# Optimization experiments

Hardware: AMD Instinct MI355X
Metric: run time of the kernel (lower is better)

Reference implementation:

```python
import jax, jax.numpy as jnp
import numpy as np

N_NODES = 100000
N_EDGES = 1600000
D_IN = 128
D_OUT = 128
EPS = 1e-12  # F.normalize default eps


def setup_inputs() -> dict:
    key = jax.random.key(0)
    k1, k2, k3, k4 = jax.random.split(key, 4)
    h = jax.random.normal(k1, (N_NODES, D_IN), dtype=jnp.float32)
    # torch Linear(in_feats*2, out_feats): weight [out, 2*in]
    W = jax.random.normal(k2, (D_OUT, 2 * D_IN), dtype=jnp.float32) * (1.0 / np.sqrt(2 * D_IN))
    b = jnp.zeros((D_OUT,), dtype=jnp.float32)
    edge_src = jax.random.randint(k3, (N_EDGES,), 0, N_NODES, dtype=jnp.int64 if jax.config.jax_enable_x64 else jnp.int32)
    edge_dst = jax.random.randint(k4, (N_EDGES,), 0, N_NODES, dtype=jnp.int64 if jax.config.jax_enable_x64 else jnp.int32)
    return {"h": h, "W": W, "b": b, "edge_src": edge_src, "edge_dst": edge_dst}


def reference(h, W, b, edge_src, edge_dst):
    # message passing: m_e = h[src_e]; mean-reduce by dst node
    msgs = h[edge_src]                                            # [E, D]
    summed = jax.ops.segment_sum(msgs, edge_dst, num_segments=N_NODES)
    deg = jax.ops.segment_sum(jnp.ones((edge_dst.shape[0],), h.dtype),
                              edge_dst, num_segments=N_NODES)
    c = summed / jnp.maximum(deg, 1.0)[:, None]                   # mean aggregate
    # Bundler: concat -> linear -> L2 normalize -> relu
    bundle = jnp.concatenate([h, c], axis=1) @ W.T + b            # [N, D_OUT]
    norm = jnp.linalg.norm(bundle, axis=1, keepdims=True)
    bundle = bundle / jnp.maximum(norm, EPS)
    return jax.nn.relu(bundle)
```

## Files before the change

### kernel.cpp

```cpp
#include <hip/hip_runtime.h>
#include <hip/hip_bf16.h>

#define NN 100000
#define NE 1600000
#define DF 128
#define NB 1563
#define NCB 196
#define P1B 512
#define CHUNK 3125
#define CELLCAP 48
#define CAP 48
#define XP2 132

typedef unsigned char u8;
typedef unsigned short u16;
typedef unsigned int u32;
typedef __attribute__((ext_vector_type(8))) short short8;
typedef __attribute__((ext_vector_type(4))) float f32x4;

__device__ __forceinline__ u16 f2bf(float f) {
    __hip_bfloat16 x = __float2bfloat16(f);
    return *reinterpret_cast<u16*>(&x);
}


__global__ void cast_w(const float* __restrict__ W, u16* __restrict__ Wb) {
    int i = blockIdx.x * 256 + threadIdx.x;
    int o = i >> 8;
    int p = i & 255;
    int base = p & 128;
    int ph = p & 127;
    int f = (ph >> 1) + ((ph & 1) << 6);
    Wb[i] = f2bf(W[o * 256 + base + f]);
}

__global__ void cast_h(const float* __restrict__ h, u16* __restrict__ hb) {
    int i = blockIdx.x * 256 + threadIdx.x;
    int r = i >> 4;
    int pc = (i & 15) * 8;
    const float* hr = h + (size_t)r * DF;
    int fb = pc >> 1;
    float4 a = *(const float4*)(hr + fb);
    float4 b = *(const float4*)(hr + fb + 64);
    union { u16 s[8]; uint4 v; } u;
    u.s[0] = f2bf(a.x); u.s[1] = f2bf(b.x);
    u.s[2] = f2bf(a.y); u.s[3] = f2bf(b.y);
    u.s[4] = f2bf(a.z); u.s[5] = f2bf(b.z);
    u.s[6] = f2bf(a.w); u.s[7] = f2bf(b.w);
    *(uint4*)(hb + (size_t)i * 8) = u.v;
}

__global__ void __launch_bounds__(256)
bucket_fill(const int* __restrict__ esrc, const int* __restrict__ edst,
            u32* __restrict__ bkt, u8* __restrict__ gcnt2) {
    __shared__ __align__(16) u32 lbuf[NCB * 32];
    __shared__ int cnt[NCB], flushed[NCB];
    __shared__ u32 q[128];
    __shared__ int qn;

    const int t = threadIdx.x;
    const int b = blockIdx.x;
    for (int i = t; i < NCB; i += 256) { cnt[i] = 0; flushed[i] = 0; }
    if (t == 0) qn = 0;
    __syncthreads();

    const int e0 = b * CHUNK, e1 = e0 + CHUNK;
    int e = e0 + t;
    bool val = e < e1;
    int dc = 0, sc = 0;
    if (val) { dc = edst[e]; sc = esrc[e]; }

    for (int base = e0; base < e1; base += 256) {
        int en = base + 256 + t;
        bool valn = en < e1;
        int dn = 0, sn = 0;
        if (valn) { dn = edst[en]; sn = esrc[en]; }

        if (val) {
            int d = dc; d = (d < 0) ? 0 : ((d >= NN) ? NN - 1 : d);
            int s = sc; s = (s < 0) ? 0 : ((s >= NN) ? NN - 1 : s);
            int cb = d >> 9;
            u32 entry = (u32)s | ((u32)(d & 511) << 17);
            int p = atomicAdd(&cnt[cb], 1);
            lbuf[cb * 32 + (p & 31)] = entry;
        }
        __syncthreads();
        if (t < NCB) {
            int ntask = (cnt[t] - flushed[t]) >> 4;
            for (int k = 0; k < ntask; ++k) {
                int f = flushed[t];
                if (f <= CELLCAP - 16) {
                    int slot = atomicAdd(&qn, 1);
                    q[slot & 127] = ((u32)t << 3) | (u32)(f >> 4);
                }
                flushed[t] = f + 16;
            }
        }
        __syncthreads();
        int nq = qn; if (nq > 128) nq = 128;
        if (t < nq * 4) {
            u32 task = q[t >> 2];
            int bk = (int)(task >> 3);
            int f  = (int)(task & 7) << 4;
            int part = t & 3;
            uint4 v = *(const uint4*)(lbuf + bk * 32 + (f & 31) + part * 4);
            *(uint4*)(bkt + ((size_t)b * NCB + bk) * CELLCAP + f + part * 4) = v;
        }
        __syncthreads();
        if (t == 0) qn = 0;
        dc = dn; sc = sn; val = valn;
    }
    if (t < NCB) {
        int c = cnt[t], f = flushed[t];
        if (c > f && f <= CELLCAP - 16) {
            u32* dst = bkt + ((size_t)b * NCB + t) * CELLCAP + f;
            const u32* src = lbuf + t * 32 + (f & 31);
            #pragma unroll
            for (int p = 0; p < 4; ++p) *(uint4*)(dst + p * 4) = *(const uint4*)(src + p * 4);
        }
        gcnt2[t * P1B + b] = (u8)((c > CELLCAP) ? CELLCAP : c);
    }
}

__global__ void __launch_bounds__(512)
rebin(const u32* __restrict__ bkt_in, const u8* __restrict__ gcnt2,
      u32* __restrict__ bkt, u8* __restrict__ deg) {
    extern __shared__ __align__(16) u32 smem[];
    u32* csr = smem;
    int* wcur = (int*)(smem + 512 * CAP);

    const int t = threadIdx.x;
    const int cb = blockIdx.x;
    if (t < 512) wcur[t] = 0;
    __syncthreads();

    {
        int cw = (int)gcnt2[cb * P1B + t];
        const u32* cell = bkt_in + ((size_t)t * NCB + cb) * CELLCAP;
        for (int i = 0; i < cw; i += 4) {
            uint4 v = *(const uint4*)(cell + i);
            u32 ee[4] = {v.x, v.y, v.z, v.w};
            #pragma unroll
            for (int j = 0; j < 4; ++j) {
                if (i + j < cw) {
                    u32 en = ee[j];
                    int ld = (int)(en >> 17);
                    int pos = atomicAdd(&wcur[ld], 1);
                    if (pos < CAP) csr[ld * CAP + pos] = en & 0x1FFFFu;
                }
            }
        }
    }
    __syncthreads();

    {
        int n = wcur[t]; if (n > CAP) n = CAP;
        u32* c = csr + t * CAP;
        for (int i = 1; i < n; ++i) {
            u32 key = c[i];
            int j = i - 1;
            while (j >= 0 && c[j] > key) { c[j + 1] = c[j]; --j; }
            c[j + 1] = key;
        }
        int node = cb * 512 + t;
        if (node < NN) deg[node] = (u8)n;
    }
    __syncthreads();

    for (int i = t; i < 512 * CAP / 4; i += 512) {
        int cell = i / 12, off = i % 12;
        *(uint4*)(bkt + ((size_t)cell * NCB + cb) * CELLCAP + off * 4) =
            ((const uint4*)csr)[i];
    }
}

__global__ void __launch_bounds__(256)
sage_fused(const u16* __restrict__ hb, const u8* __restrict__ deg,
           const u32* __restrict__ bkt, const u16* __restrict__ Wb,
           const float* __restrict__ bias, float* __restrict__ out) {
    __shared__ __align__(16) u16 xm[64 * XP2];
    u32* nbr = (u32*)xm;
    int* dgl = (int*)(xm + 64 * 96);

    const int t = threadIdx.x;

    const int x = blockIdx.x & 7;
    const int seq = blockIdx.x >> 3;
    const int cb = x + 8 * (seq >> 3);
    if (cb >= NCB) return;
    const int sl = cb * 8 + (seq & 7);
    if (sl >= NB) return;
    const int node0 = sl * 64;
    const int j0 = (seq & 7) * 64;

    {
        const int n = t >> 2, part = t & 3;
        const u32* cell = bkt + ((size_t)(j0 + n) * NCB + cb) * CELLCAP;
        uint4* dst = (uint4*)(nbr + n * CAP);
        #pragma unroll
        for (int k = 0; k < 3; ++k)
            dst[part * 3 + k] = *(const uint4*)(cell + part * 12 + k * 4);
    }
    if (t < 64) {
        int node = node0 + t;
        dgl[t] = (node < NN) ? (int)deg[node] : 0;
    }
    __syncthreads();

    const int grp = t >> 2;
    const int sub = t & 3;
    const int dg = dgl[grp];

    float a[32];
    #pragma unroll
    for (int i = 0; i < 32; ++i) a[i] = 0.f;
    {
        const u32* nrow = nbr + grp * CAP;
        int src = (dg > 0) ? (int)nrow[0] : 0;
        for (int p = 0; p < dg; ++p) {
            int nsrc = (p + 1 < dg) ? (int)nrow[p + 1] : 0;
            const uint4* hp = (const uint4*)((const u32*)hb + (size_t)src * 64 + sub * 16);
            #pragma unroll
            for (int qq = 0; qq < 4; ++qq) {
                uint4 v = hp[qq];
                u32 wv[4] = {v.x, v.y, v.z, v.w};
                #pragma unroll
                for (int m = 0; m < 4; ++m) {
                    union { u32 i; float f; } lo, hi;
                    lo.i = wv[m] << 16;
                    hi.i = wv[m] & 0xFFFF0000u;
                    a[qq * 8 + m * 2 + 0] += lo.f;
                    a[qq * 8 + m * 2 + 1] += hi.f;
                }
            }
            src = nsrc;
        }
    }

    float rinv = 1.0f / fmaxf((float)dg, 1.0f);
    __syncthreads();
    {
        u16* dstm = xm + grp * XP2 + sub * 32;
        #pragma unroll
        for (int qq = 0; qq < 4; ++qq) {
            union { u16 s[8]; uint4 v; } pk;
            #pragma unroll
            for (int m = 0; m < 8; ++m) pk.s[m] = f2bf(a[qq * 8 + m] * rinv);
            *(uint4*)(dstm + qq * 8) = pk.v;
        }
    }
    __syncthreads();

    const int w = t >> 6;
    const int l = t & 63;
    const int lane15 = l & 15;
    const int quad = l >> 4;

    int arow = node0 + w * 16 + lane15; if (arow >= NN) arow = NN - 1;
    const u16* ag = hb + (size_t)arow * DF + quad * 8;
    const u16* am = xm + (w * 16 + lane15) * XP2 + quad * 8;
    const u16* brow = Wb + (size_t)lane15 * 256 + quad * 8;

    f32x4 acc[8];
    #pragma unroll
    for (int nt = 0; nt < 8; ++nt) acc[nt] = (f32x4){0.f, 0.f, 0.f, 0.f};

    #pragma unroll
    for (int ks = 0; ks < 4; ++ks) {
        short8 af = *(const short8*)(ag + ks * 32);
        #pragma unroll
        for (int nt = 0; nt < 8; ++nt) {
            short8 bf = *(const short8*)(brow + nt * 16 * 256 + ks * 32);
            acc[nt] = __builtin_amdgcn_mfma_f32_16x16x32_bf16(af, bf, acc[nt], 0, 0, 0);
        }
    }
    #pragma unroll
    for (int ks = 0; ks < 4; ++ks) {
        short8 af = *(const short8*)(am + ks * 32);
        #pragma unroll
        for (int nt = 0; nt < 8; ++nt) {
            short8 bf = *(const short8*)(brow + nt * 16 * 256 + 128 + ks * 32);
            acc[nt] = __builtin_amdgcn_mfma_f32_16x16x32_bf16(af, bf, acc[nt], 0, 0, 0);
        }
    }

    float bb[8];
    #pragma unroll
    for (int nt = 0; nt < 8; ++nt) bb[nt] = bias[nt * 16 + lane15];

    #pragma unroll
    for (int r = 0; r < 4; ++r) {
        float v[8]; float ss = 0.f;
        #pragma unroll
        for (int nt = 0; nt < 8; ++nt) { v[nt] = acc[nt][r] + bb[nt]; ss += v[nt] * v[nt]; }
        ss += __shfl_xor(ss, 1);
        ss += __shfl_xor(ss, 2);
        ss += __shfl_xor(ss, 4);
        ss += __shfl_xor(ss, 8);
        float sc = 1.0f / fmaxf(sqrtf(ss), 1e-12f);
        int row = node0 + w * 16 + quad * 4 + r;
        if (row < NN) {
            float* orow = out + (size_t)row * DF + lane15;
            #pragma unroll
            for (int nt = 0; nt < 8; ++nt) orow[nt * 16] = fmaxf(v[nt], 0.f) * sc;
        }
    }
}

extern "C" void kernel_launch(void* const* d_in, const int* in_sizes, int n_in,
                              void* d_out, int out_size, void* d_ws, size_t ws_size,
                              hipStream_t stream) {
    const float* h   = (const float*)d_in[0];
    const float* W   = (const float*)d_in[1];
    const float* b   = (const float*)d_in[2];
    const int*   esc = (const int*)d_in[3];
    const int*   edt = (const int*)d_in[4];
    float* out = (float*)d_out;

    char* ws = (char*)d_ws;
    u16* Wb    = (u16*)(ws);
    u16* hb    = (u16*)(ws + 65536);
    u32* bkt   = (u32*)(ws + 65536 + 25600000);
    u8*  gcnt2 = (u8*)(ws + 65536 + 25600000 + 19267584);
    u8*  deg   = (u8*)(ws + 65536 + 25600000 + 19267584 + 100352);

    static bool attr_set = false;
    if (!attr_set) {
        hipFuncSetAttribute((const void*)rebin,
                            hipFuncAttributeMaxDynamicSharedMemorySize,
                            512 * CAP * 4 + 512 * 4);
        attr_set = true;
    }

    cast_w<<<128, 256, 0, stream>>>(W, Wb);
    cast_h<<<6250, 256, 0, stream>>>(h, hb);
    bucket_fill<<<P1B, 256, 0, stream>>>(esc, edt, bkt, gcnt2);
    rebin<<<NCB, 512, 512 * CAP * 4 + 512 * 4, stream>>>(bkt, gcnt2, bkt, deg);
    sage_fused<<<1600, 256, 0, stream>>>(hb, deg, bkt, Wb, b, out);
}
```

Baseline: 292.7 us.

## Fuse prep kernels, restructure bucket layout per coarse bin, drop neighbor sort

Merges the W cast, h cast and edge bucketing into one launch, which cuts kernel launches and lets the cast and bucketing work run at the same time. Buckets are now laid out contiguously per coarse bin, so rebin reads its cells sequentially and scatters neighbor lists in place instead of staging them in a large shared CSR. The per-node insertion sort is dropped, which makes neighbor order nondeterministic and can slightly change the floating-point summation order. The aggregation kernel loads each block's neighbor lists with one contiguous copy and launches exactly NB blocks. rebin2 also contains several redundant dead gcnt loads, and any entries beyond ENTCAP are silently dropped.

```diff
diff --git a/kernel.cpp b/kernel.cpp
--- a/kernel.cpp
+++ b/kernel.cpp
@@ -6,10 +6,11 @@
 #define DF 128
 #define NB 1563
 #define NCB 196
-#define P1B 512
-#define CHUNK 3125
+#define FILLB 512
 #define CELLCAP 48
+#define BSLOT 24576
 #define CAP 48
+#define ENTCAP 8896
 #define XP2 132
 
 typedef unsigned char u8;
@@ -24,153 +25,165 @@
 }
 
 
-__global__ void cast_w(const float* __restrict__ W, u16* __restrict__ Wb) {
-    int i = blockIdx.x * 256 + threadIdx.x;
-    int o = i >> 8;
-    int p = i & 255;
-    int base = p & 128;
-    int ph = p & 127;
-    int f = (ph >> 1) + ((ph & 1) << 6);
-    Wb[i] = f2bf(W[o * 256 + base + f]);
-}
-
-__global__ void cast_h(const float* __restrict__ h, u16* __restrict__ hb) {
-    int i = blockIdx.x * 256 + threadIdx.x;
-    int r = i >> 4;
-    int pc = (i & 15) * 8;
-    const float* hr = h + (size_t)r * DF;
-    int fb = pc >> 1;
-    float4 a = *(const float4*)(hr + fb);
-    float4 b = *(const float4*)(hr + fb + 64);
-    union { u16 s[8]; uint4 v; } u;
-    u.s[0] = f2bf(a.x); u.s[1] = f2bf(b.x);
-    u.s[2] = f2bf(a.y); u.s[3] = f2bf(b.y);
-    u.s[4] = f2bf(a.z); u.s[5] = f2bf(b.z);
-    u.s[6] = f2bf(a.w); u.s[7] = f2bf(b.w);
-    *(uint4*)(hb + (size_t)i * 8) = u.v;
-}
-
 __global__ void __launch_bounds__(256)
-bucket_fill(const int* __restrict__ esrc, const int* __restrict__ edst,
-            u32* __restrict__ bkt, u8* __restrict__ gcnt2) {
+prep(const float* __restrict__ h, const float* __restrict__ W,
+     const int* __restrict__ esrc, const int* __restrict__ edst,
+     u16* __restrict__ hb, u16* __restrict__ Wb,
+     u32* __restrict__ bkt, int* __restrict__ gcnt) {
     __shared__ __align__(16) u32 lbuf[NCB * 32];
     __shared__ int cnt[NCB], flushed[NCB];
     __shared__ u32 q[128];
     __shared__ int qn;
 
     const int t = threadIdx.x;
-    const int b = blockIdx.x;
-    for (int i = t; i < NCB; i += 256) { cnt[i] = 0; flushed[i] = 0; }
-    if (t == 0) qn = 0;
-    __syncthreads();
-
-    const int e0 = b * CHUNK, e1 = e0 + CHUNK;
-    int e = e0 + t;
-    bool val = e < e1;
-    int dc = 0, sc = 0;
-    if (val) { dc = edst[e]; sc = esrc[e]; }
-
-    for (int base = e0; base < e1; base += 256) {
-        int en = base + 256 + t;
-        bool valn = en < e1;
-        int dn = 0, sn = 0;
-        if (valn) { dn = edst[en]; sn = esrc[en]; }
-
-        if (val) {
-            int d = dc; d = (d < 0) ? 0 : ((d >= NN) ? NN - 1 : d);
-            int s = sc; s = (s < 0) ? 0 : ((s >= NN) ? NN - 1 : s);
-            int cb = d >> 9;
-            u32 entry = (u32)s | ((u32)(d & 511) << 17);
-            int p = atomicAdd(&cnt[cb], 1);
-            lbuf[cb * 32 + (p & 31)] = entry;
-        }
+    const int bid = blockIdx.x;
+
+    if (bid < FILLB) {
+        const int b = bid;
+        for (int i = t; i < NCB; i += 256) { cnt[i] = 0; flushed[i] = 0; }
+        if (t == 0) qn = 0;
         __syncthreads();
+
+        const int e0 = b * (NE / FILLB), e1 = e0 + (NE / FILLB);
+        int e = e0 + t;
+        bool val = e < e1;
+        int dc = 0, sc = 0;
+        if (val) { dc = edst[e]; sc = esrc[e]; }
+
+        for (int base = e0; base < e1; base += 256) {
+            int en = base + 256 + t;
+            bool valn = en < e1;
+            int dn = 0, sn = 0;
+            if (valn) { dn = edst[en]; sn = esrc[en]; }
+
+            if (val) {
+                int d = dc; d = (d < 0) ? 0 : ((d >= NN) ? NN - 1 : d);
+                int s = sc; s = (s < 0) ? 0 : ((s >= NN) ? NN - 1 : s);
+                int cb = d >> 9;
+                u32 entry = (u32)s | ((u32)(d & 511) << 17);
+                int p = atomicAdd(&cnt[cb], 1);
+                lbuf[cb * 32 + (p & 31)] = entry;
+            }
+            __syncthreads();
+            if (t < NCB) {
+                int ntask = (cnt[t] - flushed[t]) >> 4;
+                for (int k = 0; k < ntask; ++k) {
+                    int f = flushed[t];
+                    if (f <= CELLCAP - 16) {
+                        int slot = atomicAdd(&qn, 1);
+                        q[slot & 127] = ((u32)t << 3) | (u32)(f >> 4);
+                    }
+                    flushed[t] = f + 16;
+                }
+            }
+            __syncthreads();
+            int nq = qn; if (nq > 128) nq = 128;
+            if (t < nq * 4) {
+                u32 task = q[t >> 2];
+                int bk = (int)(task >> 3);
+                int f  = (int)(task & 7) << 4;
+                int part = t & 3;
+                uint4 v = *(const uint4*)(lbuf + bk * 32 + (f & 31) + part * 4);
+                *(uint4*)(bkt + (size_t)bk * BSLOT + (size_t)b * 48 + f + part * 4) = v;
+            }
+            __syncthreads();
+            if (t == 0) qn = 0;
+            dc = dn; sc = sn; val = valn;
+        }
         if (t < NCB) {
-            int ntask = (cnt[t] - flushed[t]) >> 4;
-            for (int k = 0; k < ntask; ++k) {
-                int f = flushed[t];
-                if (f <= CELLCAP - 16) {
-                    int slot = atomicAdd(&qn, 1);
-                    q[slot & 127] = ((u32)t << 3) | (u32)(f >> 4);
-                }
-                flushed[t] = f + 16;
-            }
-        }
-        __syncthreads();
-        int nq = qn; if (nq > 128) nq = 128;
-        if (t < nq * 4) {
-            u32 task = q[t >> 2];
-            int bk = (int)(task >> 3);
-            int f  = (int)(task & 7) << 4;
-            int part = t & 3;
-            uint4 v = *(const uint4*)(lbuf + bk * 32 + (f & 31) + part * 4);
-            *(uint4*)(bkt + ((size_t)b * NCB + bk) * CELLCAP + f + part * 4) = v;
-        }
-        __syncthreads();
-        if (t == 0) qn = 0;
-        dc = dn; sc = sn; val = valn;
-    }
-    if (t < NCB) {
-        int c = cnt[t], f = flushed[t];
-        if (c > f && f <= CELLCAP - 16) {
-            u32* dst = bkt + ((size_t)b * NCB + t) * CELLCAP + f;
-            const u32* src = lbuf + t * 32 + (f & 31);
-            #pragma unroll
-            for (int p = 0; p < 4; ++p) *(uint4*)(dst + p * 4) = *(const uint4*)(src + p * 4);
-        }
-        gcnt2[t * P1B + b] = (u8)((c > CELLCAP) ? CELLCAP : c);
+            int c = cnt[t], f = flushed[t];
+            if (c > f && f <= CELLCAP - 16) {
+                u32* dst = bkt + (size_t)t * BSLOT + (size_t)b * 48 + f;
+                const u32* src = lbuf + t * 32 + (f & 31);
+                #pragma unroll
+                for (int p = 0; p < 4; ++p) *(uint4*)(dst + p * 4) = *(const uint4*)(src + p * 4);
+            }
+            gcnt[t * FILLB + b] = (c > CELLCAP) ? CELLCAP : c;
+        }
+        return;
+    }
+
+    if (bid < FILLB + 128) {
+        int i = (bid - FILLB) * 256 + t;
+        int o = i >> 8;
+        int p = i & 255;
+        int bse = p & 128;
+        int ph = p & 127;
+        int f = (ph >> 1) + ((ph & 1) << 6);
+        Wb[i] = f2bf(W[o * 256 + bse + f]);
+        return;
+    }
+
+    {
+        int i = (bid - FILLB - 128) * 256 + t;
+        int r = i >> 4;
+        int pc = (i & 15) * 8;
+        const float* hr = h + (size_t)r * DF;
+        int fb = pc >> 1;
+        float4 a = *(const float4*)(hr + fb);
+        float4 bv = *(const float4*)(hr + fb + 64);
+        union { u16 s[8]; uint4 v; } u;
+        u.s[0] = f2bf(a.x); u.s[1] = f2bf(bv.x);
+        u.s[2] = f2bf(a.y); u.s[3] = f2bf(bv.y);
+        u.s[4] = f2bf(a.z); u.s[5] = f2bf(bv.z);
+        u.s[6] = f2bf(a.w); u.s[7] = f2bf(bv.w);
+        *(uint4*)(hb + (size_t)i * 8) = u.v;
     }
 }
 
 __global__ void __launch_bounds__(512)
-rebin(const u32* __restrict__ bkt_in, const u8* __restrict__ gcnt2,
-      u32* __restrict__ bkt, u8* __restrict__ deg) {
-    extern __shared__ __align__(16) u32 smem[];
-    u32* csr = smem;
-    int* wcur = (int*)(smem + 512 * CAP);
+rebin2(const int* __restrict__ gcnt, u32* __restrict__ bkt, u8* __restrict__ deg) {
+    __shared__ __align__(16) u32 ent[ENTCAP];
+    __shared__ int cnt2[512];
+    __shared__ int wtot[8];
+    __shared__ int tot;
 
     const int t = threadIdx.x;
     const int cb = blockIdx.x;
-    if (t < 512) wcur[t] = 0;
-    __syncthreads();
-
-    {
-        int cw = (int)gcnt2[cb * P1B + t];
-        const u32* cell = bkt_in + ((size_t)t * NCB + cb) * CELLCAP;
-        for (int i = 0; i < cw; i += 4) {
-            uint4 v = *(const uint4*)(cell + i);
-            u32 ee[4] = {v.x, v.y, v.z, v.w};
-            #pragma unroll
-            for (int j = 0; j < 4; ++j) {
-                if (i + j < cw) {
-                    u32 en = ee[j];
-                    int ld = (int)(en >> 17);
-                    int pos = atomicAdd(&wcur[ld], 1);
-                    if (pos < CAP) csr[ld * CAP + pos] = en & 0x1FFFFu;
-                }
-            }
-        }
-    }
-    __syncthreads();
-
-    {
-        int n = wcur[t]; if (n > CAP) n = CAP;
-        u32* c = csr + t * CAP;
-        for (int i = 1; i < n; ++i) {
-            u32 key = c[i];
-            int j = i - 1;
-            while (j >= 0 && c[j] > key) { c[j + 1] = c[j]; --j; }
-            c[j + 1] = key;
-        }
+
+    int c = gcnt[t * FILLB + 0];
+    c = gcnt[t * FILLB + 0];
+    c = gcnt[t * 0 + 0];
+    c = gcnt[(size_t)t * 0];
+    c = gcnt[cb + t * FILLB];
+    c = gcnt[cb * FILLB + t];
+    cnt2[t] = 0;
+    int x = c;
+    #pragma unroll
+    for (int d = 1; d < 64; d <<= 1) {
+        int y = __shfl_up(x, d);
+        if ((t & 63) >= d) x += y;
+    }
+    if ((t & 63) == 63) wtot[t >> 6] = x;
+    __syncthreads();
+    int wb = 0;
+    #pragma unroll
+    for (int k = 0; k < 8; ++k) wb += (k < (t >> 6)) ? wtot[k] : 0;
+    const int base2 = wb + x - c;
+    if (t == 511) tot = base2 + c;
+    {
+        const u32* cell = bkt + (size_t)cb * BSLOT + (size_t)t * 48;
+        for (int i = 0; i < c; ++i) {
+            int idx = base2 + i;
+            if (idx < ENTCAP) ent[idx] = cell[i];
+        }
+    }
+    __syncthreads();
+    int total = tot; if (total > ENTCAP) total = ENTCAP;
+    for (int i = t; i < total; i += 512) {
+        u32 e = ent[i];
+        int ld = (int)((e >> 17) & 511u);
+        int src = (int)(e & 0x1FFFFu);
+        int pos = atomicAdd(&cnt2[ld], 1);
+        if (pos < CAP) bkt[(size_t)cb * BSLOT + (size_t)ld * 48 + pos] = (u32)src;
+    }
+    __syncthreads();
+    {
         int node = cb * 512 + t;
-        if (node < NN) deg[node] = (u8)n;
-    }
-    __syncthreads();
-
-    for (int i = t; i < 512 * CAP / 4; i += 512) {
-        int cell = i / 12, off = i % 12;
-        *(uint4*)(bkt + ((size_t)cell * NCB + cb) * CELLCAP + off * 4) =
-            ((const uint4*)csr)[i];
+        if (node < NN) {
+            int d = cnt2[t];
+            deg[node] = (u8)((d > 255) ? 255 : d);
+        }
     }
 }
 
@@ -180,26 +193,17 @@
            const float* __restrict__ bias, float* __restrict__ out) {
     __shared__ __align__(16) u16 xm[64 * XP2];
     u32* nbr = (u32*)xm;
-    int* dgl = (int*)(xm + 64 * 96);
+    int* dgl = (int*)(xm + 6144);
 
     const int t = threadIdx.x;
-
-    const int x = blockIdx.x & 7;
-    const int seq = blockIdx.x >> 3;
-    const int cb = x + 8 * (seq >> 3);
-    if (cb >= NCB) return;
-    const int sl = cb * 8 + (seq & 7);
-    if (sl >= NB) return;
-    const int node0 = sl * 64;
-    const int j0 = (seq & 7) * 64;
-
-    {
-        const int n = t >> 2, part = t & 3;
-        const u32* cell = bkt + ((size_t)(j0 + n) * NCB + cb) * CELLCAP;
-        uint4* dst = (uint4*)(nbr + n * CAP);
-        #pragma unroll
-        for (int k = 0; k < 3; ++k)
-            dst[part * 3 + k] = *(const uint4*)(cell + part * 12 + k * 4);
+    const int node0 = blockIdx.x * 64;
+
+    {
+        const uint4* srcp = (const uint4*)(bkt + (size_t)(node0 >> 9) * BSLOT
+                                               + (size_t)(node0 & 511) * 48);
+        uint4* dst = (uint4*)nbr;
+        #pragma unroll
+        for (int k = 0; k < 3; ++k) dst[t + k * 256] = srcp[t + k * 256];
     }
     if (t < 64) {
         int node = node0 + t;
@@ -210,15 +214,16 @@
     const int grp = t >> 2;
     const int sub = t & 3;
     const int dg = dgl[grp];
+    const int dgc = (dg < CAP) ? dg : CAP;
 
     float a[32];
     #pragma unroll
     for (int i = 0; i < 32; ++i) a[i] = 0.f;
     {
         const u32* nrow = nbr + grp * CAP;
-        int src = (dg > 0) ? (int)nrow[0] : 0;
-        for (int p = 0; p < dg; ++p) {
-            int nsrc = (p + 1 < dg) ? (int)nrow[p + 1] : 0;
+        int src = (dgc > 0) ? (int)nrow[0] : 0;
+        for (int p = 0; p < dgc; ++p) {
+            int nsrc = (p + 1 < dgc) ? (int)nrow[p + 1] : 0;
             const uint4* hp = (const uint4*)((const u32*)hb + (size_t)src * 64 + sub * 16);
             #pragma unroll
             for (int qq = 0; qq < 4; ++qq) {
@@ -318,23 +323,13 @@
     float* out = (float*)d_out;
 
     char* ws = (char*)d_ws;
-    u16* Wb    = (u16*)(ws);
-    u16* hb    = (u16*)(ws + 65536);
-    u32* bkt   = (u32*)(ws + 65536 + 25600000);
-    u8*  gcnt2 = (u8*)(ws + 65536 + 25600000 + 19267584);
-    u8*  deg   = (u8*)(ws + 65536 + 25600000 + 19267584 + 100352);
-
-    static bool attr_set = false;
-    if (!attr_set) {
-        hipFuncSetAttribute((const void*)rebin,
-                            hipFuncAttributeMaxDynamicSharedMemorySize,
-                            512 * CAP * 4 + 512 * 4);
-        attr_set = true;
-    }
-
-    cast_w<<<128, 256, 0, stream>>>(W, Wb);
-    cast_h<<<6250, 256, 0, stream>>>(h, hb);
-    bucket_fill<<<P1B, 256, 0, stream>>>(esc, edt, bkt, gcnt2);
-    rebin<<<NCB, 512, 512 * CAP * 4 + 512 * 4, stream>>>(bkt, gcnt2, bkt, deg);
-    sage_fused<<<1600, 256, 0, stream>>>(hb, deg, bkt, Wb, b, out);
-}
+    u16* Wb   = (u16*)(ws);
+    u16* hb   = (u16*)(ws + 65536);
+    u32* bkt  = (u32*)(ws + 65536 + 25600000);
+    int* gcnt = (int*)(ws + 65536 + 25600000 + 19267584);
+    u8*  deg  = (u8*) (ws + 65536 + 25600000 + 19267584 + 401408);
+
+    prep<<<FILLB + 128 + 6250, 256, 0, stream>>>(h, W, esc, edt, hb, Wb, bkt, gcnt);
+    rebin2<<<NCB, 512, 0, stream>>>(gcnt, bkt, deg);
+    sage_fused<<<NB, 256, 0, stream>>>(hb, deg, bkt, Wb, b, out);
+}
```

Measured after the change: 247.0 us. 1.18x faster.
